# Optimization experiments

Hardware: AMD Instinct MI355X
Metric: run time of the kernel (lower is better)

## Reference

```python
import jax, jax.numpy as jnp
import numpy as np

B, S, E, H = 1, 4096, 1024, 16
HD = E // H  # 64


def setup_inputs() -> dict:
    key = jax.random.key(0)
    ks = jax.random.split(key, 5)
    scale = 0.02
    x = jax.random.normal(ks[0], (B, S, E), dtype=jnp.float32)
    # per-head Q/K/V weights, nn.Linear convention: W[out, in]
    wq = jax.random.normal(ks[1], (H, HD, HD), dtype=jnp.float32) * scale
    wk = jax.random.normal(ks[2], (H, HD, HD), dtype=jnp.float32) * scale
    wv = jax.random.normal(ks[3], (H, HD, HD), dtype=jnp.float32) * scale
    wo = jax.random.normal(ks[4], (E, E), dtype=jnp.float32) * scale
    return {"x": x, "wq": wq, "wk": wk, "wv": wv, "wo": wo}


def reference(x, wq, wk, wv, wo):
    b, s, e = x.shape
    h, hd = wq.shape[0], wq.shape[1]
    xh = x.reshape(b, s, h, hd)
    # per-head linear: y = x @ W^T  (W is [out, in])
    q = jnp.einsum('bshd,hod->bsho', xh, wq)
    k = jnp.einsum('bshd,hod->bsho', xh, wk)
    v = jnp.einsum('bshd,hod->bsho', xh, wv)
    scores = jnp.einsum('bqho,bkho->bhqk', q, k) / jnp.sqrt(jnp.float32(hd))
    causal = jnp.tril(jnp.ones((s, s), dtype=bool))  # [S, S]
    scores = jnp.where(causal, scores, -jnp.inf)
    weights = jax.nn.softmax(scores, axis=-1)
    out = jnp.einsum('bhqk,bkho->bqho', weights, v).reshape(b, s, h * hd)
    return out @ wo.T
```

## Files before the change

kernel.cpp:

```cpp
#include <hip/hip_runtime.h>
#include <hip/hip_bf16.h>

typedef __bf16 bf16;
typedef __bf16 bf16x8 __attribute__((ext_vector_type(8)));
typedef __bf16 bf16x4 __attribute__((ext_vector_type(4)));
typedef float f32x4 __attribute__((ext_vector_type(4)));

#define MFMA16(a, b, c) __builtin_amdgcn_mfma_f32_16x16x32_bf16((a), (b), (c), 0, 0, 0)

constexpr int S = 4096;
constexpr int E = 1024;
constexpr int H = 16;
constexpr int HD = 64;
constexpr float NEG = -1e30f;
constexpr float QSCALE = 0.125f * 1.44269504088896f;

__device__ inline bf16x8 load_f32x8_as_bf16(const float* __restrict__ p) {
  float4 u0 = *reinterpret_cast<const float4*>(p);
  float4 u1 = *reinterpret_cast<const float4*>(p + 4);
  bf16x8 r;
  r[0] = (bf16)u0.x; r[1] = (bf16)u0.y; r[2] = (bf16)u0.z; r[3] = (bf16)u0.w;
  r[4] = (bf16)u1.x; r[5] = (bf16)u1.y; r[6] = (bf16)u1.z; r[7] = (bf16)u1.w;
  return r;
}

__global__ __launch_bounds__(256) void qkv_cvt_kernel(
    const float* __restrict__ x, const float* __restrict__ wq,
    const float* __restrict__ wk, const float* __restrict__ wv,
    const float* __restrict__ wo,
    bf16* __restrict__ qb, bf16* __restrict__ kb, bf16* __restrict__ vt,
    bf16* __restrict__ wob) {
  if (blockIdx.y == 16) {
    for (int i = (blockIdx.x * 256 + threadIdx.x) * 4; i < E * E; i += 64 * 256 * 4) {
      float4 f = *reinterpret_cast<const float4*>(wo + i);
      bf16x4 b;
      b[0] = (bf16)f.x; b[1] = (bf16)f.y; b[2] = (bf16)f.z; b[3] = (bf16)f.w;
      *reinterpret_cast<bf16x4*>(wob + i) = b;
    }
    return;
  }
  const int h = blockIdx.y;
  const int s0 = blockIdx.x * 64;
  const int w = threadIdx.x >> 6;
  const int l = threadIdx.x & 63;
  const int lg = l >> 4, lr = l & 15;

  bf16x8 af[2];
  {
    const float* xp = x + (size_t)(s0 + w * 16 + lr) * E + h * HD;
    af[0] = load_f32x8_as_bf16(xp + lg * 8);
    af[1] = load_f32x8_as_bf16(xp + 32 + lg * 8);
  }
  const float* Wsrc[3] = {wq + (size_t)h * HD * HD, wk + (size_t)h * HD * HD,
                          wv + (size_t)h * HD * HD};
#pragma unroll
  for (int pj = 0; pj < 3; ++pj) {
    f32x4 acc[4];
#pragma unroll
    for (int ot = 0; ot < 4; ++ot) acc[ot] = f32x4{0.f, 0.f, 0.f, 0.f};
#pragma unroll
    for (int ks = 0; ks < 2; ++ks) {
#pragma unroll
      for (int ot = 0; ot < 4; ++ot) {
        bf16x8 bfr = load_f32x8_as_bf16(Wsrc[pj] + (size_t)(ot * 16 + lr) * HD + ks * 32 + lg * 8);
        acc[ot] = MFMA16(af[ks], bfr, acc[ot]);
      }
    }
    if (pj == 2) {
#pragma unroll
      for (int ot = 0; ot < 4; ++ot) {
        bf16x4 b;
#pragma unroll
        for (int r = 0; r < 4; ++r) b[r] = (bf16)acc[ot][r];
        *reinterpret_cast<bf16x4*>(vt + (size_t)(h * HD + ot * 16 + lr) * S +
                                   s0 + w * 16 + lg * 4) = b;
      }
    } else {
      const float scale = (pj == 0) ? QSCALE : 1.0f;
      bf16* op = ((pj == 0) ? qb : kb) + (size_t)h * S * HD;
#pragma unroll
      for (int ot = 0; ot < 4; ++ot)
#pragma unroll
        for (int r = 0; r < 4; ++r)
          op[(size_t)(s0 + w * 16 + lg * 4 + r) * HD + ot * 16 + lr] =
              (bf16)(acc[ot][r] * scale);
    }
  }
}

__global__ __launch_bounds__(256, 4) void attn_kernel(
    const bf16* __restrict__ qb, const bf16* __restrict__ kb,
    const bf16* __restrict__ vt, bf16* __restrict__ ob) {
  __shared__ bf16 Kl[2][64 * 64];
  __shared__ bf16 Vl[2][64 * 64];
  const int b = blockIdx.x;
  const int xcd = b & 7;
  const int idx = b >> 3;
  const int p = idx >> 1, hb = idx & 1;
  const int head = 2 * xcd + hb;
  const int qt = (p < 32) ? (hb ? p : 63 - p) : (hb ? 95 - p : p - 32);
  const int tid = threadIdx.x;
  const int w = tid >> 6, l = tid & 63;
  const int qc = l & 15, h = l >> 4;
  const int q0w = qt * 64 + w * 16;
  const int nst = qt + 1;

  bf16x8 qf[2];
  {
    const bf16* qp = qb + ((size_t)head * S + q0w + qc) * HD + h * 8;
    qf[0] = *reinterpret_cast<const bf16x8*>(qp);
    qf[1] = *reinterpret_cast<const bf16x8*>(qp + 32);
  }
  const bf16* kbase = kb + (size_t)head * S * HD;
  const bf16* vbase = vt + (size_t)head * HD * S;

  f32x4 acc[4];
#pragma unroll
  for (int i = 0; i < 4; ++i) acc[i] = f32x4{0.f, 0.f, 0.f, 0.f};
  float mrun = NEG, lsum = 0.f;

  auto gload = [&](int st, bf16x8 (&kr)[2], bf16x8 (&vr)[2]) {
    const int kv0 = st * 64;
#pragma unroll
    for (int j = 0; j < 2; ++j) {
      const int g = tid + j * 256;
      const int row = g >> 3, ge = g & 7;
      kr[j] = *reinterpret_cast<const bf16x8*>(kbase + (size_t)(kv0 + row) * HD + ge * 8);
      vr[j] = *reinterpret_cast<const bf16x8*>(vbase + (size_t)row * S + kv0 + ge * 8);
    }
  };
  auto swrite = [&](int buf, bf16x8 (&kr)[2], bf16x8 (&vr)[2]) {
#pragma unroll
    for (int j = 0; j < 2; ++j) {
      const int g = tid + j * 256;
      const int row = g >> 3, ge = g & 7;
      const int off = row * 64 + ((ge * 8) ^ ((row & 7) << 3));
      *reinterpret_cast<bf16x8*>(&Kl[buf][off]) = kr[j];
      *reinterpret_cast<bf16x8*>(&Vl[buf][off]) = vr[j];
    }
  };

  bf16x8 kr[2], vr[2];
  gload(0, kr, vr);
  swrite(0, kr, vr);
  __syncthreads();

  for (int st = 0; st < nst; ++st) {
    const int buf = st & 1;
    const int kv0 = st * 64;
    const bool pre = (st + 1 < nst);
    if (pre) gload(st + 1, kr, vr);

    if (kv0 <= q0w + 15) {
      f32x4 sv[4];
#pragma unroll
      for (int t = 0; t < 4; ++t) sv[t] = f32x4{0.f, 0.f, 0.f, 0.f};
      __builtin_amdgcn_s_setprio(1);
#pragma unroll
      for (int c = 0; c < 2; ++c)
#pragma unroll
        for (int t = 0; t < 4; ++t) {
          bf16x8 kf = *reinterpret_cast<const bf16x8*>(
              &Kl[buf][(16 * t + qc) * 64 + ((c * 32 + h * 8) ^ ((qc & 7) << 3))]);
          sv[t] = MFMA16(kf, qf[c], sv[t]);
        }
      __builtin_amdgcn_s_setprio(0);
      if (kv0 + 63 > q0w) {
        const int q = q0w + qc;
#pragma unroll
        for (int t = 0; t < 4; ++t)
#pragma unroll
          for (int r = 0; r < 4; ++r)
            if (kv0 + 16 * t + 4 * h + r > q) sv[t][r] = NEG;
      }
      float tmax = NEG;
#pragma unroll
      for (int t = 0; t < 4; ++t)
#pragma unroll
        for (int r = 0; r < 4; ++r) tmax = fmaxf(tmax, sv[t][r]);
      if (!__all(tmax <= mrun + 8.f)) {
        float tm = fmaxf(tmax, __shfl_xor(tmax, 16));
        tm = fmaxf(tm, __shfl_xor(tm, 32));
        float mnew = fmaxf(mrun, tm);
        float alpha = exp2f(mrun - mnew);
        lsum *= alpha;
#pragma unroll
        for (int dt = 0; dt < 4; ++dt)
#pragma unroll
          for (int r = 0; r < 4; ++r) acc[dt][r] *= alpha;
        mrun = mnew;
      }
      float psum = 0.f;
#pragma unroll
      for (int t = 0; t < 4; ++t)
#pragma unroll
        for (int r = 0; r < 4; ++r) {
          float d = sv[t][r] - mrun;
          float e;
          asm("v_exp_f32 %0, %1" : "=v"(e) : "v"(d));
          sv[t][r] = e;
          psum += e;
        }
      lsum += psum;
      unsigned pk[4][2];
#pragma unroll
      for (int t = 0; t < 4; ++t) {
        union { unsigned u; bf16 h2[2]; } a, bqq;
        a.h2[0] = (bf16)sv[t][0]; a.h2[1] = (bf16)sv[t][1];
        bqq.h2[0] = (bf16)sv[t][2]; bqq.h2[1] = (bf16)sv[t][3];
        pk[t][0] = a.u; pk[t][1] = bqq.u;
      }
#pragma unroll
      for (int c2 = 0; c2 < 2; ++c2) {
        unsigned x0 = pk[2 * c2][0], y0 = pk[2 * c2 + 1][0];
        unsigned x1 = pk[2 * c2][1], y1 = pk[2 * c2 + 1][1];
        asm("v_permlane32_swap_b32 %0, %1" : "+v"(x0), "+v"(y0));
        asm("v_permlane16_swap_b32 %0, %1" : "+v"(x0), "+v"(y0));
        asm("v_permlane32_swap_b32 %0, %1" : "+v"(x1), "+v"(y1));
        asm("v_permlane16_swap_b32 %0, %1" : "+v"(x1), "+v"(y1));
        union { bf16x8 v; unsigned u[4]; } B;
        B.u[0] = x0; B.u[1] = x1; B.u[2] = y0; B.u[3] = y1;
        __builtin_amdgcn_s_setprio(1);
#pragma unroll
        for (int dt = 0; dt < 4; ++dt) {
          bf16x8 vf = *reinterpret_cast<const bf16x8*>(
              &Vl[buf][(16 * dt + qc) * 64 + ((c2 * 32 + h * 8) ^ ((qc & 7) << 3))]);
          acc[dt] = MFMA16(vf, B.v, acc[dt]);
        }
        __builtin_amdgcn_s_setprio(0);
      }
    }
    if (pre) swrite(buf ^ 1, kr, vr);
    __syncthreads();
  }

  float lt = lsum + __shfl_xor(lsum, 16);
  lt += __shfl_xor(lt, 32);
  const float inv = 1.0f / lt;
  bf16* obp = ob + (size_t)(q0w + qc) * E + head * HD;
#pragma unroll
  for (int dt = 0; dt < 4; ++dt) {
    bf16x4 bb;
#pragma unroll
    for (int r = 0; r < 4; ++r) bb[r] = (bf16)(acc[dt][r] * inv);
    *reinterpret_cast<bf16x4*>(obp + 16 * dt + 4 * h) = bb;
  }
}

__global__ __launch_bounds__(256) void out_gemm_kernel(
    const bf16* __restrict__ ob, const bf16* __restrict__ wob,
    float* __restrict__ out) {
  __shared__ bf16 Bl[2][128 * 64];
  const int tid = threadIdx.x;
  const int w = tid >> 6, l = tid & 63, lg = l >> 4, lr = l & 15;
  const int s0 = blockIdx.x * 128, e0 = blockIdx.y * 128;
  f32x4 acc[2][8];
#pragma unroll
  for (int rt = 0; rt < 2; ++rt)
#pragma unroll
    for (int ct = 0; ct < 8; ++ct) acc[rt][ct] = f32x4{0.f, 0.f, 0.f, 0.f};
  const bf16* ap0 = ob + (size_t)(s0 + w * 32 + lr) * E;
  const bf16* ap1 = ap0 + (size_t)16 * E;

  auto gloadB = [&](int k0, bf16x8 (&br)[4]) {
#pragma unroll
    for (int j = 0; j < 4; ++j) {
      const int g = tid + j * 256;
      const int col = g >> 3, ge = g & 7;
      br[j] = *reinterpret_cast<const bf16x8*>(wob + (size_t)(e0 + col) * E + k0 + ge * 8);
    }
  };
  auto swriteB = [&](int buf, bf16x8 (&br)[4]) {
#pragma unroll
    for (int j = 0; j < 4; ++j) {
      const int g = tid + j * 256;
      const int col = g >> 3, ge = g & 7;
      *reinterpret_cast<bf16x8*>(&Bl[buf][col * 64 + ((ge * 8) ^ ((col & 7) << 3))]) = br[j];
    }
  };

  bf16x8 br[4];
  gloadB(0, br);
  swriteB(0, br);
  __syncthreads();

  for (int it = 0; it < 16; ++it) {
    const int k0 = it * 64;
    const int buf = it & 1;
    const bool pre = (it + 1 < 16);
    if (pre) gloadB(k0 + 64, br);

    bf16x8 af[2][2];
#pragma unroll
    for (int ks = 0; ks < 2; ++ks) {
      af[0][ks] = *reinterpret_cast<const bf16x8*>(ap0 + k0 + ks * 32 + lg * 8);
      af[1][ks] = *reinterpret_cast<const bf16x8*>(ap1 + k0 + ks * 32 + lg * 8);
    }
#pragma unroll
    for (int ks = 0; ks < 2; ++ks)
#pragma unroll
      for (int ct = 0; ct < 8; ++ct) {
        bf16x8 bfr = *reinterpret_cast<const bf16x8*>(
            &Bl[buf][(ct * 16 + lr) * 64 + ((ks * 32 + lg * 8) ^ ((lr & 7) << 3))]);
        acc[0][ct] = MFMA16(af[0][ks], bfr, acc[0][ct]);
        acc[1][ct] = MFMA16(af[1][ks], bfr, acc[1][ct]);
      }
    if (pre) swriteB(buf ^ 1, br);
    __syncthreads();
  }

#pragma unroll
  for (int rt = 0; rt < 2; ++rt)
#pragma unroll
    for (int ct = 0; ct < 8; ++ct)
#pragma unroll
      for (int r = 0; r < 4; ++r)
        out[(size_t)(s0 + w * 32 + rt * 16 + lg * 4 + r) * E + e0 + ct * 16 + lr] =
            acc[rt][ct][r];
}

extern "C" void kernel_launch(void* const* d_in, const int* in_sizes, int n_in,
                              void* d_out, int out_size, void* d_ws, size_t ws_size,
                              hipStream_t stream) {
  const float* x  = (const float*)d_in[0];
  const float* wq = (const float*)d_in[1];
  const float* wk = (const float*)d_in[2];
  const float* wv = (const float*)d_in[3];
  const float* wo = (const float*)d_in[4];
  float* out = (float*)d_out;

  bf16* qb  = (bf16*)d_ws;
  bf16* kb  = qb + (size_t)H * S * HD;
  bf16* vt  = kb + (size_t)H * S * HD;
  bf16* ob  = vt + (size_t)H * S * HD;
  bf16* wob = ob + (size_t)S * E;

  qkv_cvt_kernel<<<dim3(S / 64, H + 1), 256, 0, stream>>>(x, wq, wk, wv, wo, qb, kb, vt, wob);
  attn_kernel<<<dim3(1024), 256, 0, stream>>>(qb, kb, vt, ob);
  out_gemm_kernel<<<dim3(S / 128, E / 128), 256, 0, stream>>>(ob, wob, out);
}
```

Before: 130.4 us.

## Split attention KV tile across warp pairs with 32-row query blocks and merge

Each warp now handles 32 query rows against half of the 64-key tile, rather than 16 query rows against the full tile. Each K fragment loaded from LDS is reused for two query subtiles, and each V fragment for two accumulators, which cuts LDS reads per MFMA. The two key-halves keep separate online-softmax states. These are merged at the end through shared memory, which adds an extra sync plus LDS traffic and raises register pressure.

```diff
diff --git a/kernel.cpp b/kernel.cpp
--- a/kernel.cpp
+++ b/kernel.cpp
@@ -102,41 +102,48 @@
   const int tid = threadIdx.x;
   const int w = tid >> 6, l = tid & 63;
   const int qc = l & 15, h = l >> 4;
-  const int q0w = qt * 64 + w * 16;
+  const int i = w & 1, j = w >> 1;
+  const int j32 = j * 32;
+  const int q0w = qt * 64 + i * 32;
   const int nst = qt + 1;
-
-  bf16x8 qf[2];
+  const int sw = (qc & 7) << 3;
+
+  bf16x8 qf[2][2];
   {
     const bf16* qp = qb + ((size_t)head * S + q0w + qc) * HD + h * 8;
-    qf[0] = *reinterpret_cast<const bf16x8*>(qp);
-    qf[1] = *reinterpret_cast<const bf16x8*>(qp + 32);
+    qf[0][0] = *reinterpret_cast<const bf16x8*>(qp);
+    qf[0][1] = *reinterpret_cast<const bf16x8*>(qp + 32);
+    qf[1][0] = *reinterpret_cast<const bf16x8*>(qp + 16 * HD);
+    qf[1][1] = *reinterpret_cast<const bf16x8*>(qp + 16 * HD + 32);
   }
   const bf16* kbase = kb + (size_t)head * S * HD;
   const bf16* vbase = vt + (size_t)head * HD * S;
 
-  f32x4 acc[4];
-#pragma unroll
-  for (int i = 0; i < 4; ++i) acc[i] = f32x4{0.f, 0.f, 0.f, 0.f};
-  float mrun = NEG, lsum = 0.f;
+  f32x4 acc[2][4];
+#pragma unroll
+  for (int u = 0; u < 2; ++u)
+#pragma unroll
+    for (int dt = 0; dt < 4; ++dt) acc[u][dt] = f32x4{0.f, 0.f, 0.f, 0.f};
+  float m0 = NEG, m1 = NEG, l0 = 0.f, l1 = 0.f;
 
   auto gload = [&](int st, bf16x8 (&kr)[2], bf16x8 (&vr)[2]) {
     const int kv0 = st * 64;
 #pragma unroll
-    for (int j = 0; j < 2; ++j) {
-      const int g = tid + j * 256;
+    for (int jj = 0; jj < 2; ++jj) {
+      const int g = tid + jj * 256;
       const int row = g >> 3, ge = g & 7;
-      kr[j] = *reinterpret_cast<const bf16x8*>(kbase + (size_t)(kv0 + row) * HD + ge * 8);
-      vr[j] = *reinterpret_cast<const bf16x8*>(vbase + (size_t)row * S + kv0 + ge * 8);
+      kr[jj] = *reinterpret_cast<const bf16x8*>(kbase + (size_t)(kv0 + row) * HD + ge * 8);
+      vr[jj] = *reinterpret_cast<const bf16x8*>(vbase + (size_t)row * S + kv0 + ge * 8);
     }
   };
   auto swrite = [&](int buf, bf16x8 (&kr)[2], bf16x8 (&vr)[2]) {
 #pragma unroll
-    for (int j = 0; j < 2; ++j) {
-      const int g = tid + j * 256;
+    for (int jj = 0; jj < 2; ++jj) {
+      const int g = tid + jj * 256;
       const int row = g >> 3, ge = g & 7;
       const int off = row * 64 + ((ge * 8) ^ ((row & 7) << 3));
-      *reinterpret_cast<bf16x8*>(&Kl[buf][off]) = kr[j];
-      *reinterpret_cast<bf16x8*>(&Vl[buf][off]) = vr[j];
+      *reinterpret_cast<bf16x8*>(&Kl[buf][off]) = kr[jj];
+      *reinterpret_cast<bf16x8*>(&Vl[buf][off]) = vr[jj];
     }
   };
 
@@ -151,82 +158,97 @@
     const bool pre = (st + 1 < nst);
     if (pre) gload(st + 1, kr, vr);
 
-    if (kv0 <= q0w + 15) {
-      f32x4 sv[4];
-#pragma unroll
-      for (int t = 0; t < 4; ++t) sv[t] = f32x4{0.f, 0.f, 0.f, 0.f};
+    if (kv0 + j32 <= q0w + 31) {
+      bf16x8 kf[2][2];
+#pragma unroll
+      for (int t = 0; t < 2; ++t)
+#pragma unroll
+        for (int c = 0; c < 2; ++c)
+          kf[t][c] = *reinterpret_cast<const bf16x8*>(
+              &Kl[buf][(j32 + 16 * t + qc) * 64 + ((c * 32 + h * 8) ^ sw)]);
+      f32x4 sv[2][2];
       __builtin_amdgcn_s_setprio(1);
 #pragma unroll
-      for (int c = 0; c < 2; ++c)
-#pragma unroll
-        for (int t = 0; t < 4; ++t) {
-          bf16x8 kf = *reinterpret_cast<const bf16x8*>(
-              &Kl[buf][(16 * t + qc) * 64 + ((c * 32 + h * 8) ^ ((qc & 7) << 3))]);
-          sv[t] = MFMA16(kf, qf[c], sv[t]);
+      for (int u = 0; u < 2; ++u)
+#pragma unroll
+        for (int t = 0; t < 2; ++t) {
+          f32x4 a = f32x4{0.f, 0.f, 0.f, 0.f};
+          a = MFMA16(kf[t][0], qf[u][0], a);
+          a = MFMA16(kf[t][1], qf[u][1], a);
+          sv[u][t] = a;
         }
       __builtin_amdgcn_s_setprio(0);
+      bf16x8 vf[4];
+#pragma unroll
+      for (int dt = 0; dt < 4; ++dt)
+        vf[dt] = *reinterpret_cast<const bf16x8*>(
+            &Vl[buf][(16 * dt + qc) * 64 + ((j32 + h * 8) ^ sw)]);
       if (kv0 + 63 > q0w) {
-        const int q = q0w + qc;
-#pragma unroll
-        for (int t = 0; t < 4; ++t)
-#pragma unroll
-          for (int r = 0; r < 4; ++r)
-            if (kv0 + 16 * t + 4 * h + r > q) sv[t][r] = NEG;
-      }
-      float tmax = NEG;
-#pragma unroll
-      for (int t = 0; t < 4; ++t)
-#pragma unroll
-        for (int r = 0; r < 4; ++r) tmax = fmaxf(tmax, sv[t][r]);
-      if (!__all(tmax <= mrun + 8.f)) {
-        float tm = fmaxf(tmax, __shfl_xor(tmax, 16));
-        tm = fmaxf(tm, __shfl_xor(tm, 32));
-        float mnew = fmaxf(mrun, tm);
-        float alpha = exp2f(mrun - mnew);
-        lsum *= alpha;
+#pragma unroll
+        for (int u = 0; u < 2; ++u) {
+          const int q = q0w + u * 16 + qc;
+#pragma unroll
+          for (int t = 0; t < 2; ++t)
+#pragma unroll
+            for (int r = 0; r < 4; ++r)
+              if (kv0 + j32 + 16 * t + 4 * h + r > q) sv[u][t][r] = NEG;
+        }
+      }
+      float t0 = NEG, t1 = NEG;
+#pragma unroll
+      for (int t = 0; t < 2; ++t)
+#pragma unroll
+        for (int r = 0; r < 4; ++r) {
+          t0 = fmaxf(t0, sv[0][t][r]);
+          t1 = fmaxf(t1, sv[1][t][r]);
+        }
+      if (!__all((t0 <= m0 + 8.f) && (t1 <= m1 + 8.f))) {
+        float a0 = fmaxf(t0, __shfl_xor(t0, 16));
+        a0 = fmaxf(a0, __shfl_xor(a0, 32));
+        float a1 = fmaxf(t1, __shfl_xor(t1, 16));
+        a1 = fmaxf(a1, __shfl_xor(a1, 32));
+        float mn0 = fmaxf(m0, a0), mn1 = fmaxf(m1, a1);
+        float al0 = exp2f(m0 - mn0), al1 = exp2f(m1 - mn1);
+        l0 *= al0; l1 *= al1;
 #pragma unroll
         for (int dt = 0; dt < 4; ++dt)
 #pragma unroll
-          for (int r = 0; r < 4; ++r) acc[dt][r] *= alpha;
-        mrun = mnew;
-      }
-      float psum = 0.f;
-#pragma unroll
-      for (int t = 0; t < 4; ++t)
+          for (int r = 0; r < 4; ++r) {
+            acc[0][dt][r] *= al0;
+            acc[1][dt][r] *= al1;
+          }
+        m0 = mn0; m1 = mn1;
+      }
+      float p0 = 0.f, p1 = 0.f;
+#pragma unroll
+      for (int t = 0; t < 2; ++t)
 #pragma unroll
         for (int r = 0; r < 4; ++r) {
-          float d = sv[t][r] - mrun;
-          float e;
-          asm("v_exp_f32 %0, %1" : "=v"(e) : "v"(d));
-          sv[t][r] = e;
-          psum += e;
-        }
-      lsum += psum;
-      unsigned pk[4][2];
-#pragma unroll
-      for (int t = 0; t < 4; ++t) {
-        union { unsigned u; bf16 h2[2]; } a, bqq;
-        a.h2[0] = (bf16)sv[t][0]; a.h2[1] = (bf16)sv[t][1];
-        bqq.h2[0] = (bf16)sv[t][2]; bqq.h2[1] = (bf16)sv[t][3];
-        pk[t][0] = a.u; pk[t][1] = bqq.u;
-      }
-#pragma unroll
-      for (int c2 = 0; c2 < 2; ++c2) {
-        unsigned x0 = pk[2 * c2][0], y0 = pk[2 * c2 + 1][0];
-        unsigned x1 = pk[2 * c2][1], y1 = pk[2 * c2 + 1][1];
+          float d0 = sv[0][t][r] - m0, e0;
+          asm("v_exp_f32 %0, %1" : "=v"(e0) : "v"(d0));
+          sv[0][t][r] = e0; p0 += e0;
+          float d1 = sv[1][t][r] - m1, e1;
+          asm("v_exp_f32 %0, %1" : "=v"(e1) : "v"(d1));
+          sv[1][t][r] = e1; p1 += e1;
+        }
+      l0 += p0; l1 += p1;
+#pragma unroll
+      for (int u = 0; u < 2; ++u) {
+        union { unsigned u32; bf16 h2[2]; } pa, pb;
+        unsigned x0, x1, y0, y1;
+        pa.h2[0] = (bf16)sv[u][0][0]; pa.h2[1] = (bf16)sv[u][0][1]; x0 = pa.u32;
+        pb.h2[0] = (bf16)sv[u][0][2]; pb.h2[1] = (bf16)sv[u][0][3]; x1 = pb.u32;
+        pa.h2[0] = (bf16)sv[u][1][0]; pa.h2[1] = (bf16)sv[u][1][1]; y0 = pa.u32;
+        pb.h2[0] = (bf16)sv[u][1][2]; pb.h2[1] = (bf16)sv[u][1][3]; y1 = pb.u32;
         asm("v_permlane32_swap_b32 %0, %1" : "+v"(x0), "+v"(y0));
         asm("v_permlane16_swap_b32 %0, %1" : "+v"(x0), "+v"(y0));
         asm("v_permlane32_swap_b32 %0, %1" : "+v"(x1), "+v"(y1));
         asm("v_permlane16_swap_b32 %0, %1" : "+v"(x1), "+v"(y1));
-        union { bf16x8 v; unsigned u[4]; } B;
-        B.u[0] = x0; B.u[1] = x1; B.u[2] = y0; B.u[3] = y1;
+        union { bf16x8 v; unsigned uu[4]; } B;
+        B.uu[0] = x0; B.uu[1] = x1; B.uu[2] = y0; B.uu[3] = y1;
         __builtin_amdgcn_s_setprio(1);
 #pragma unroll
-        for (int dt = 0; dt < 4; ++dt) {
-          bf16x8 vf = *reinterpret_cast<const bf16x8*>(
-              &Vl[buf][(16 * dt + qc) * 64 + ((c2 * 32 + h * 8) ^ ((qc & 7) << 3))]);
-          acc[dt] = MFMA16(vf, B.v, acc[dt]);
-        }
+        for (int dt = 0; dt < 4; ++dt) acc[u][dt] = MFMA16(vf[dt], B.v, acc[u][dt]);
         __builtin_amdgcn_s_setprio(0);
       }
     }
@@ -234,16 +256,48 @@
     __syncthreads();
   }
 
-  float lt = lsum + __shfl_xor(lsum, 16);
-  lt += __shfl_xor(lt, 32);
-  const float inv = 1.0f / lt;
-  bf16* obp = ob + (size_t)(q0w + qc) * E + head * HD;
-#pragma unroll
-  for (int dt = 0; dt < 4; ++dt) {
-    bf16x4 bb;
-#pragma unroll
-    for (int r = 0; r < 4; ++r) bb[r] = (bf16)(acc[dt][r] * inv);
-    *reinterpret_cast<bf16x4*>(obp + 16 * dt + 4 * h) = bb;
+  float lt0 = l0 + __shfl_xor(l0, 16); lt0 += __shfl_xor(lt0, 32);
+  float lt1 = l1 + __shfl_xor(l1, 16); lt1 += __shfl_xor(lt1, 32);
+
+  float* fK = (float*)Kl;
+  float* fV = (float*)Vl;
+  if (j == 1) {
+#pragma unroll
+    for (int u = 0; u < 2; ++u) {
+#pragma unroll
+      for (int dt = 0; dt < 4; ++dt)
+#pragma unroll
+        for (int r = 0; r < 4; ++r)
+          fK[((((i * 2 + u) * 4 + dt) * 4 + h) * 4 + r) * 16 + qc] = acc[u][dt][r];
+      if (h == 0) {
+        fV[((i * 2 + u) * 16 + qc) * 2] = (u == 0) ? m0 : m1;
+        fV[((i * 2 + u) * 16 + qc) * 2 + 1] = (u == 0) ? lt0 : lt1;
+      }
+    }
+  }
+  __syncthreads();
+  if (j == 0) {
+#pragma unroll
+    for (int u = 0; u < 2; ++u) {
+      const float mA = (u == 0) ? m0 : m1;
+      const float lA = (u == 0) ? lt0 : lt1;
+      const float mB = fV[((i * 2 + u) * 16 + qc) * 2];
+      const float lB = fV[((i * 2 + u) * 16 + qc) * 2 + 1];
+      const float M = fmaxf(mA, mB);
+      const float eA = exp2f(mA - M), eB = exp2f(mB - M);
+      const float inv = 1.0f / (eA * lA + eB * lB);
+      bf16* obp = ob + (size_t)(q0w + u * 16 + qc) * E + head * HD;
+#pragma unroll
+      for (int dt = 0; dt < 4; ++dt) {
+        bf16x4 bb;
+#pragma unroll
+        for (int r = 0; r < 4; ++r) {
+          float vB = fK[((((i * 2 + u) * 4 + dt) * 4 + h) * 4 + r) * 16 + qc];
+          bb[r] = (bf16)((eA * acc[u][dt][r] + eB * vB) * inv);
+        }
+        *reinterpret_cast<bf16x4*>(obp + 16 * dt + 4 * h) = bb;
+      }
+    }
   }
 }
 
@@ -264,18 +318,18 @@
 
   auto gloadB = [&](int k0, bf16x8 (&br)[4]) {
 #pragma unroll
-    for (int j = 0; j < 4; ++j) {
-      const int g = tid + j * 256;
+    for (int jj = 0; jj < 4; ++jj) {
+      const int g = tid + jj * 256;
       const int col = g >> 3, ge = g & 7;
-      br[j] = *reinterpret_cast<const bf16x8*>(wob + (size_t)(e0 + col) * E + k0 + ge * 8);
+      br[jj] = *reinterpret_cast<const bf16x8*>(wob + (size_t)(e0 + col) * E + k0 + ge * 8);
     }
   };
   auto swriteB = [&](int buf, bf16x8 (&br)[4]) {
 #pragma unroll
-    for (int j = 0; j < 4; ++j) {
-      const int g = tid + j * 256;
+    for (int jj = 0; jj < 4; ++jj) {
+      const int g = tid + jj * 256;
       const int col = g >> 3, ge = g & 7;
-      *reinterpret_cast<bf16x8*>(&Bl[buf][col * 64 + ((ge * 8) ^ ((col & 7) << 3))]) = br[j];
+      *reinterpret_cast<bf16x8*>(&Bl[buf][col * 64 + ((ge * 8) ^ ((col & 7) << 3))]) = br[jj];
     }
   };
 
```

New measurement: 125.2 us. -4.0%, faster.

## Pair complementary causal query tiles per block and split KV across warp halves

Applied to the files above, without the earlier changes.

Each attention block now takes two query tiles (qt and 63-qt), so every block does the same amount of causal work, and it shares one K/V shared-memory load between both tiles. Blocks grow to 512 threads. The two warp groups each take half of every 64-key tile, split-K style, and their partial softmax states are merged through shared memory at the end. This is meant to balance the causal workload and halve the K/V staging traffic per query. In exchange it adds a combine step with extra syncs, more registers for two accumulator sets, and the 512-thread launch bound may reduce occupancy.

```diff
diff --git a/kernel.cpp b/kernel.cpp
--- a/kernel.cpp
+++ b/kernel.cpp
@@ -88,7 +88,7 @@
   }
 }
 
-__global__ __launch_bounds__(256, 4) void attn_kernel(
+__global__ __launch_bounds__(512, 2) void attn_kernel(
     const bf16* __restrict__ qb, const bf16* __restrict__ kb,
     const bf16* __restrict__ vt, bf16* __restrict__ ob) {
   __shared__ bf16 Kl[2][64 * 64];
@@ -98,152 +98,195 @@
   const int idx = b >> 3;
   const int p = idx >> 1, hb = idx & 1;
   const int head = 2 * xcd + hb;
-  const int qt = (p < 32) ? (hb ? p : 63 - p) : (hb ? 95 - p : p - 32);
+  const int qt5 = (p < 16) ? (hb ? p : 31 - p) : (hb ? 47 - p : p - 16);
+  const int qtA = 32 + qt5;
+  const int qtB = 63 - qtA;
   const int tid = threadIdx.x;
   const int w = tid >> 6, l = tid & 63;
   const int qc = l & 15, h = l >> 4;
-  const int q0w = qt * 64 + w * 16;
-  const int nst = qt + 1;
-
-  bf16x8 qf[2];
+  const int i2 = w & 3, j = w >> 2;
+  const int j32 = j * 32;
+  const int q0A = qtA * 64 + i2 * 16;
+  const int q0B = qtB * 64 + i2 * 16;
+  const int nst = qtA + 1;
+  const int sw = (qc & 7) << 3;
+
+  bf16x8 qfA[2], qfB[2];
   {
-    const bf16* qp = qb + ((size_t)head * S + q0w + qc) * HD + h * 8;
-    qf[0] = *reinterpret_cast<const bf16x8*>(qp);
-    qf[1] = *reinterpret_cast<const bf16x8*>(qp + 32);
+    const bf16* qpA = qb + ((size_t)head * S + q0A + qc) * HD + h * 8;
+    qfA[0] = *reinterpret_cast<const bf16x8*>(qpA);
+    qfA[1] = *reinterpret_cast<const bf16x8*>(qpA + 32);
+    const bf16* qpB = qb + ((size_t)head * S + q0B + qc) * HD + h * 8;
+    qfB[0] = *reinterpret_cast<const bf16x8*>(qpB);
+    qfB[1] = *reinterpret_cast<const bf16x8*>(qpB + 32);
   }
   const bf16* kbase = kb + (size_t)head * S * HD;
   const bf16* vbase = vt + (size_t)head * HD * S;
 
-  f32x4 acc[4];
-#pragma unroll
-  for (int i = 0; i < 4; ++i) acc[i] = f32x4{0.f, 0.f, 0.f, 0.f};
-  float mrun = NEG, lsum = 0.f;
-
-  auto gload = [&](int st, bf16x8 (&kr)[2], bf16x8 (&vr)[2]) {
-    const int kv0 = st * 64;
-#pragma unroll
-    for (int j = 0; j < 2; ++j) {
-      const int g = tid + j * 256;
-      const int row = g >> 3, ge = g & 7;
-      kr[j] = *reinterpret_cast<const bf16x8*>(kbase + (size_t)(kv0 + row) * HD + ge * 8);
-      vr[j] = *reinterpret_cast<const bf16x8*>(vbase + (size_t)row * S + kv0 + ge * 8);
-    }
-  };
-  auto swrite = [&](int buf, bf16x8 (&kr)[2], bf16x8 (&vr)[2]) {
-#pragma unroll
-    for (int j = 0; j < 2; ++j) {
-      const int g = tid + j * 256;
-      const int row = g >> 3, ge = g & 7;
-      const int off = row * 64 + ((ge * 8) ^ ((row & 7) << 3));
-      *reinterpret_cast<bf16x8*>(&Kl[buf][off]) = kr[j];
-      *reinterpret_cast<bf16x8*>(&Vl[buf][off]) = vr[j];
-    }
-  };
-
-  bf16x8 kr[2], vr[2];
-  gload(0, kr, vr);
-  swrite(0, kr, vr);
+  f32x4 accA[4], accB[4];
+#pragma unroll
+  for (int dt = 0; dt < 4; ++dt) {
+    accA[dt] = f32x4{0.f, 0.f, 0.f, 0.f};
+    accB[dt] = f32x4{0.f, 0.f, 0.f, 0.f};
+  }
+  float mA = NEG, lA = 0.f, mB = NEG, lB = 0.f;
+
+  auto gload = [&](int st, bf16x8& kr, bf16x8& vr) {
+    const int kv0s = st * 64;
+    const int row = tid >> 3, ge = tid & 7;
+    kr = *reinterpret_cast<const bf16x8*>(kbase + (size_t)(kv0s + row) * HD + ge * 8);
+    vr = *reinterpret_cast<const bf16x8*>(vbase + (size_t)row * S + kv0s + ge * 8);
+  };
+  auto swrite = [&](int buf, bf16x8& kr, bf16x8& vr) {
+    const int row = tid >> 3, ge = tid & 7;
+    const int off = row * 64 + ((ge * 8) ^ ((row & 7) << 3));
+    *reinterpret_cast<bf16x8*>(&Kl[buf][off]) = kr;
+    *reinterpret_cast<bf16x8*>(&Vl[buf][off]) = vr;
+  };
+
+  auto tileStep = [&](int q0, const bf16x8 (&qf)[2], f32x4 (&acc)[4], float& m, float& ls,
+                      const bf16x8 (&kf)[2][2], const bf16x8 (&vf)[4], int kv0) {
+    f32x4 sv[2];
+    __builtin_amdgcn_s_setprio(1);
+#pragma unroll
+    for (int t = 0; t < 2; ++t) {
+      f32x4 a = f32x4{0.f, 0.f, 0.f, 0.f};
+      a = MFMA16(kf[t][0], qf[0], a);
+      a = MFMA16(kf[t][1], qf[1], a);
+      sv[t] = a;
+    }
+    __builtin_amdgcn_s_setprio(0);
+    if (kv0 + 63 > q0) {
+      const int q = q0 + qc;
+#pragma unroll
+      for (int t = 0; t < 2; ++t)
+#pragma unroll
+        for (int r = 0; r < 4; ++r)
+          if (kv0 + j32 + 16 * t + 4 * h + r > q) sv[t][r] = NEG;
+    }
+    float tmax = NEG;
+#pragma unroll
+    for (int t = 0; t < 2; ++t)
+#pragma unroll
+      for (int r = 0; r < 4; ++r) tmax = fmaxf(tmax, sv[t][r]);
+    if (!__all(tmax <= m + 8.f)) {
+      float tm = fmaxf(tmax, __shfl_xor(tmax, 16));
+      tm = fmaxf(tm, __shfl_xor(tm, 32));
+      float mnew = fmaxf(m, tm);
+      float alpha = exp2f(m - mnew);
+      ls *= alpha;
+#pragma unroll
+      for (int dt = 0; dt < 4; ++dt)
+#pragma unroll
+        for (int r = 0; r < 4; ++r) acc[dt][r] *= alpha;
+      m = mnew;
+    }
+    float psum = 0.f;
+#pragma unroll
+    for (int t = 0; t < 2; ++t)
+#pragma unroll
+      for (int r = 0; r < 4; ++r) {
+        float d = sv[t][r] - m, e;
+        asm("v_exp_f32 %0, %1" : "=v"(e) : "v"(d));
+        sv[t][r] = e;
+        psum += e;
+      }
+    ls += psum;
+    union { unsigned u32; bf16 h2[2]; } pa, pb;
+    unsigned x0, x1, y0, y1;
+    pa.h2[0] = (bf16)sv[0][0]; pa.h2[1] = (bf16)sv[0][1]; x0 = pa.u32;
+    pb.h2[0] = (bf16)sv[0][2]; pb.h2[1] = (bf16)sv[0][3]; x1 = pb.u32;
+    pa.h2[0] = (bf16)sv[1][0]; pa.h2[1] = (bf16)sv[1][1]; y0 = pa.u32;
+    pb.h2[0] = (bf16)sv[1][2]; pb.h2[1] = (bf16)sv[1][3]; y1 = pb.u32;
+    asm("v_permlane32_swap_b32 %0, %1" : "+v"(x0), "+v"(y0));
+    asm("v_permlane16_swap_b32 %0, %1" : "+v"(x0), "+v"(y0));
+    asm("v_permlane32_swap_b32 %0, %1" : "+v"(x1), "+v"(y1));
+    asm("v_permlane16_swap_b32 %0, %1" : "+v"(x1), "+v"(y1));
+    union { bf16x8 v; unsigned uu[4]; } B;
+    B.uu[0] = x0; B.uu[1] = x1; B.uu[2] = y0; B.uu[3] = y1;
+    __builtin_amdgcn_s_setprio(1);
+#pragma unroll
+    for (int dt = 0; dt < 4; ++dt) acc[dt] = MFMA16(vf[dt], B.v, acc[dt]);
+    __builtin_amdgcn_s_setprio(0);
+  };
+
+  {
+    bf16x8 kr, vr;
+    gload(0, kr, vr);
+    swrite(0, kr, vr);
+  }
   __syncthreads();
 
   for (int st = 0; st < nst; ++st) {
     const int buf = st & 1;
     const int kv0 = st * 64;
     const bool pre = (st + 1 < nst);
+    bf16x8 kr, vr;
     if (pre) gload(st + 1, kr, vr);
 
-    if (kv0 <= q0w + 15) {
-      f32x4 sv[4];
-#pragma unroll
-      for (int t = 0; t < 4; ++t) sv[t] = f32x4{0.f, 0.f, 0.f, 0.f};
-      __builtin_amdgcn_s_setprio(1);
-#pragma unroll
-      for (int c = 0; c < 2; ++c)
-#pragma unroll
-        for (int t = 0; t < 4; ++t) {
-          bf16x8 kf = *reinterpret_cast<const bf16x8*>(
-              &Kl[buf][(16 * t + qc) * 64 + ((c * 32 + h * 8) ^ ((qc & 7) << 3))]);
-          sv[t] = MFMA16(kf, qf[c], sv[t]);
-        }
-      __builtin_amdgcn_s_setprio(0);
-      if (kv0 + 63 > q0w) {
-        const int q = q0w + qc;
-#pragma unroll
-        for (int t = 0; t < 4; ++t)
-#pragma unroll
-          for (int r = 0; r < 4; ++r)
-            if (kv0 + 16 * t + 4 * h + r > q) sv[t][r] = NEG;
-      }
-      float tmax = NEG;
-#pragma unroll
-      for (int t = 0; t < 4; ++t)
-#pragma unroll
-        for (int r = 0; r < 4; ++r) tmax = fmaxf(tmax, sv[t][r]);
-      if (!__all(tmax <= mrun + 8.f)) {
-        float tm = fmaxf(tmax, __shfl_xor(tmax, 16));
-        tm = fmaxf(tm, __shfl_xor(tm, 32));
-        float mnew = fmaxf(mrun, tm);
-        float alpha = exp2f(mrun - mnew);
-        lsum *= alpha;
-#pragma unroll
-        for (int dt = 0; dt < 4; ++dt)
-#pragma unroll
-          for (int r = 0; r < 4; ++r) acc[dt][r] *= alpha;
-        mrun = mnew;
-      }
-      float psum = 0.f;
-#pragma unroll
-      for (int t = 0; t < 4; ++t)
-#pragma unroll
-        for (int r = 0; r < 4; ++r) {
-          float d = sv[t][r] - mrun;
-          float e;
-          asm("v_exp_f32 %0, %1" : "=v"(e) : "v"(d));
-          sv[t][r] = e;
-          psum += e;
-        }
-      lsum += psum;
-      unsigned pk[4][2];
-#pragma unroll
-      for (int t = 0; t < 4; ++t) {
-        union { unsigned u; bf16 h2[2]; } a, bqq;
-        a.h2[0] = (bf16)sv[t][0]; a.h2[1] = (bf16)sv[t][1];
-        bqq.h2[0] = (bf16)sv[t][2]; bqq.h2[1] = (bf16)sv[t][3];
-        pk[t][0] = a.u; pk[t][1] = bqq.u;
-      }
-#pragma unroll
-      for (int c2 = 0; c2 < 2; ++c2) {
-        unsigned x0 = pk[2 * c2][0], y0 = pk[2 * c2 + 1][0];
-        unsigned x1 = pk[2 * c2][1], y1 = pk[2 * c2 + 1][1];
-        asm("v_permlane32_swap_b32 %0, %1" : "+v"(x0), "+v"(y0));
-        asm("v_permlane16_swap_b32 %0, %1" : "+v"(x0), "+v"(y0));
-        asm("v_permlane32_swap_b32 %0, %1" : "+v"(x1), "+v"(y1));
-        asm("v_permlane16_swap_b32 %0, %1" : "+v"(x1), "+v"(y1));
-        union { bf16x8 v; unsigned u[4]; } B;
-        B.u[0] = x0; B.u[1] = x1; B.u[2] = y0; B.u[3] = y1;
-        __builtin_amdgcn_s_setprio(1);
-#pragma unroll
-        for (int dt = 0; dt < 4; ++dt) {
-          bf16x8 vf = *reinterpret_cast<const bf16x8*>(
-              &Vl[buf][(16 * dt + qc) * 64 + ((c2 * 32 + h * 8) ^ ((qc & 7) << 3))]);
-          acc[dt] = MFMA16(vf, B.v, acc[dt]);
-        }
-        __builtin_amdgcn_s_setprio(0);
-      }
+    const bool actA = (kv0 + j32 <= q0A + 15);
+    const bool actB = (kv0 + j32 <= q0B + 15);
+    if (actA || actB) {
+      bf16x8 kf[2][2], vf[4];
+#pragma unroll
+      for (int t = 0; t < 2; ++t)
+#pragma unroll
+        for (int c = 0; c < 2; ++c)
+          kf[t][c] = *reinterpret_cast<const bf16x8*>(
+              &Kl[buf][(j32 + 16 * t + qc) * 64 + ((c * 32 + h * 8) ^ sw)]);
+#pragma unroll
+      for (int dt = 0; dt < 4; ++dt)
+        vf[dt] = *reinterpret_cast<const bf16x8*>(
+            &Vl[buf][(16 * dt + qc) * 64 + ((j32 + h * 8) ^ sw)]);
+      if (actA) tileStep(q0A, qfA, accA, mA, lA, kf, vf, kv0);
+      if (actB) tileStep(q0B, qfB, accB, mB, lB, kf, vf, kv0);
     }
     if (pre) swrite(buf ^ 1, kr, vr);
     __syncthreads();
   }
 
-  float lt = lsum + __shfl_xor(lsum, 16);
-  lt += __shfl_xor(lt, 32);
-  const float inv = 1.0f / lt;
-  bf16* obp = ob + (size_t)(q0w + qc) * E + head * HD;
-#pragma unroll
-  for (int dt = 0; dt < 4; ++dt) {
-    bf16x4 bb;
-#pragma unroll
-    for (int r = 0; r < 4; ++r) bb[r] = (bf16)(acc[dt][r] * inv);
-    *reinterpret_cast<bf16x4*>(obp + 16 * dt + 4 * h) = bb;
+  float ltA = lA + __shfl_xor(lA, 16); ltA += __shfl_xor(ltA, 32);
+  float ltB = lB + __shfl_xor(lB, 16); ltB += __shfl_xor(ltB, 32);
+
+  float* fK = (float*)Kl;
+  float* fV = (float*)Vl;
+#pragma unroll
+  for (int ph = 0; ph < 2; ++ph) {
+    f32x4* acc = (ph == 0) ? accA : accB;
+    const float mS = (ph == 0) ? mA : mB;
+    const float lS = (ph == 0) ? ltA : ltB;
+    const int q0 = (ph == 0) ? q0A : q0B;
+    if (j == 1) {
+#pragma unroll
+      for (int dt = 0; dt < 4; ++dt)
+#pragma unroll
+        for (int r = 0; r < 4; ++r)
+          fK[(((i2 * 4 + dt) * 4 + h) * 4 + r) * 16 + qc] = acc[dt][r];
+      if (h == 0) {
+        fV[(i2 * 16 + qc) * 2] = mS;
+        fV[(i2 * 16 + qc) * 2 + 1] = lS;
+      }
+    }
+    __syncthreads();
+    if (j == 0) {
+      const float mO = fV[(i2 * 16 + qc) * 2];
+      const float lO = fV[(i2 * 16 + qc) * 2 + 1];
+      const float M = fmaxf(mS, mO);
+      const float eA = exp2f(mS - M), eB = exp2f(mO - M);
+      const float inv = 1.0f / (eA * lS + eB * lO);
+      bf16* obp = ob + (size_t)(q0 + qc) * E + head * HD;
+#pragma unroll
+      for (int dt = 0; dt < 4; ++dt) {
+        bf16x4 bb;
+#pragma unroll
+        for (int r = 0; r < 4; ++r) {
+          float vB = fK[(((i2 * 4 + dt) * 4 + h) * 4 + r) * 16 + qc];
+          bb[r] = (bf16)((eA * acc[dt][r] + eB * vB) * inv);
+        }
+        *reinterpret_cast<bf16x4*>(obp + 16 * dt + 4 * h) = bb;
+      }
+    }
+    __syncthreads();
   }
 }
 
@@ -264,18 +307,18 @@
 
   auto gloadB = [&](int k0, bf16x8 (&br)[4]) {
 #pragma unroll
-    for (int j = 0; j < 4; ++j) {
-      const int g = tid + j * 256;
+    for (int jj = 0; jj < 4; ++jj) {
+      const int g = tid + jj * 256;
       const int col = g >> 3, ge = g & 7;
-      br[j] = *reinterpret_cast<const bf16x8*>(wob + (size_t)(e0 + col) * E + k0 + ge * 8);
+      br[jj] = *reinterpret_cast<const bf16x8*>(wob + (size_t)(e0 + col) * E + k0 + ge * 8);
     }
   };
   auto swriteB = [&](int buf, bf16x8 (&br)[4]) {
 #pragma unroll
-    for (int j = 0; j < 4; ++j) {
-      const int g = tid + j * 256;
+    for (int jj = 0; jj < 4; ++jj) {
+      const int g = tid + jj * 256;
       const int col = g >> 3, ge = g & 7;
-      *reinterpret_cast<bf16x8*>(&Bl[buf][col * 64 + ((ge * 8) ^ ((col & 7) << 3))]) = br[j];
+      *reinterpret_cast<bf16x8*>(&Bl[buf][col * 64 + ((ge * 8) ^ ((col & 7) << 3))]) = br[jj];
     }
   };
 
@@ -336,6 +379,6 @@
   bf16* wob = ob + (size_t)S * E;
 
   qkv_cvt_kernel<<<dim3(S / 64, H + 1), 256, 0, stream>>>(x, wq, wk, wv, wo, qb, kb, vt, wob);
-  attn_kernel<<<dim3(1024), 256, 0, stream>>>(qb, kb, vt, ob);
+  attn_kernel<<<dim3(512), 512, 0, stream>>>(qb, kb, vt, ob);
   out_gemm_kernel<<<dim3(S / 128, E / 128), 256, 0, stream>>>(ob, wob, out);
 }
```

After: 142.9 us. 9.6% more time.
